# Kernel tuning notes

Measured on AMD Instinct MI355X. Metric: run time of the kernel, lower is better.

Reference implementation:

```python
import jax, jax.numpy as jnp
import numpy as np
import math

B, C, A, W, H = 8, 128, 16, 64, 64


def setup_inputs() -> dict:
    key = jax.random.key(0)
    ks = jax.random.split(key, 7)
    s_in = 1.0 / math.sqrt(C)
    return {
        "x": jax.random.normal(ks[0], (B, C, W, H), dtype=jnp.float32),
        "Wq": jax.random.normal(ks[1], (A, C), dtype=jnp.float32) * s_in,
        "bq": jnp.zeros((A,), dtype=jnp.float32),
        "Wk": jax.random.normal(ks[2], (A, C), dtype=jnp.float32) * s_in,
        "bk": jnp.zeros((A,), dtype=jnp.float32),
        "Wv": jax.random.normal(ks[3], (C, C), dtype=jnp.float32) * s_in,
        "bv": jnp.zeros((C,), dtype=jnp.float32),
    }


def reference(x, Wq, bq, Wk, bk, Wv, bv):
    # 1x1 convs == per-pixel linear projections
    q = jnp.einsum('ac,bcwh->bawh', Wq, x) + bq[None, :, None, None]  # [B,A,W,H]
    k = jnp.einsum('ac,bcwh->bawh', Wk, x) + bk[None, :, None, None]  # [B,A,W,H]
    v = jnp.einsum('vc,bcwh->bvwh', Wv, x) + bv[None, :, None, None]  # [B,C,W,H]

    scale = 1.0 / math.sqrt(q.shape[1])
    # full spatial attention: [B, W, H, W, H]
    attn = jnp.einsum('bawh,baWH->bwhWH', q, k)
    b, w, h, _, _ = attn.shape
    attn = jax.nn.softmax(attn.reshape(b, w, h, -1) * scale, axis=-1)
    attn = attn.reshape(b, w, h, w, h)
    out = jnp.einsum('bwhWH,bvWH->bvwh', attn, v)  # [B,C,W,H]
    return out
```

## Files before the change

### kernel.cpp

```cpp
#include <hip/hip_runtime.h>
#include <math.h>

#define BB 8
#define CC 128
#define NN 4096

typedef _Float16 f16;
typedef _Float16 f16x4v __attribute__((ext_vector_type(4)));
typedef _Float16 f16x8 __attribute__((ext_vector_type(8)));
typedef float f32x4v __attribute__((ext_vector_type(4)));
typedef float f32x16 __attribute__((ext_vector_type(16)));

#if __has_builtin(__builtin_amdgcn_exp2f)
#define EXP2(x) __builtin_amdgcn_exp2f(x)
#else
#define EXP2(x) __expf((x)*0.69314718056f)
#endif

#define QSCALE 0.360673760222f
#define SHIFT  5.770780163555f

#define WF_BYTES 65536

__global__ __launch_bounds__(256)
void prep_kernel(const float* __restrict__ Wq, const float* __restrict__ bq,
                 const float* __restrict__ Wk, const float* __restrict__ bk,
                 const float* __restrict__ Wv, const float* __restrict__ bv,
                 f16* __restrict__ Wf, float* __restrict__ biasS)
{
    const int tg = blockIdx.x*256 + threadIdx.x;
    if (tg < 2560) {
        const int mt = tg >> 9, ks = (tg >> 6) & 7, l = tg & 63;
        const int n32 = l & 31, h = l >> 5;
        const int r = mt*32 + n32;
        f16x8 v8;
        #pragma unroll
        for (int i = 0; i < 8; i++) {
            int c = ks*16 + 8*h + i;
            float wv_;
            if (r < 16)      wv_ = QSCALE * Wq[r*CC + c];
            else if (r < 32) wv_ = Wk[(r-16)*CC + c];
            else             wv_ = Wv[(r-32)*CC + c];
            v8[i] = (f16)wv_;
        }
        *(f16x8*)&Wf[(size_t)tg*8] = v8;
    }
    if (blockIdx.x == 0 && threadIdx.x < 160) {
        int r = threadIdx.x;
        biasS[r] = r < 16 ? QSCALE*bq[r] : (r < 32 ? bk[r-16] : bv[r-32]);
    }
}

__global__ __launch_bounds__(256)
void proj_kernel(const float* __restrict__ x, const f16* __restrict__ Wf,
                 const float* __restrict__ biasS,
                 f16* __restrict__ Qt, f16* __restrict__ Kt, f16* __restrict__ Vf)
{
    __shared__ __align__(16) f16 Vl[CC*140];

    const int tid  = threadIdx.x;
    const int lane = tid & 63;
    const int wv   = tid >> 6;
    const int b    = blockIdx.x & 7;
    const int pt   = blockIdx.x >> 3;
    const int n32  = lane & 31;
    const int half = lane >> 5;
    const int p    = pt*128 + wv*32 + n32;

    const float* xp = x + (size_t)b*CC*NN + p;
    f16x8 xf[8];
    #pragma unroll
    for (int ks = 0; ks < 8; ks++) {
        float xv[8];
        #pragma unroll
        for (int i = 0; i < 8; i++)
            xv[i] = __builtin_nontemporal_load(&xp[(size_t)(ks*16 + 8*half + i)*NN]);
        #pragma unroll
        for (int i = 0; i < 8; i++) xf[ks][i] = (f16)xv[i];
    }

    f32x16 acc[5];
    #pragma unroll
    for (int mt = 0; mt < 5; mt++) acc[mt] = (f32x16)0.0f;
    #pragma unroll
    for (int ks = 0; ks < 8; ks++) {
        #pragma unroll
        for (int mt = 0; mt < 5; mt++) {
            f16x8 wfr = *(const f16x8*)&Wf[((size_t)(mt*8 + ks)*64 + lane)*8];
            acc[mt] = __builtin_amdgcn_mfma_f32_32x32x16_f16(wfr, xf[ks], acc[mt], 0, 0, 0);
        }
    }

    #pragma unroll
    for (int mt = 0; mt < 5; mt++) {
        #pragma unroll
        for (int q = 0; q < 4; q++) {
            float4 b4 = *(const float4*)&biasS[mt*32 + q*8 + 4*half];
            acc[mt][q*4+0] += b4.x; acc[mt][q*4+1] += b4.y;
            acc[mt][q*4+2] += b4.z; acc[mt][q*4+3] += b4.w;
        }
    }

    {
        size_t qkoff = ((size_t)b*NN + p)*16;
        f16x4v s0, s1, s2, s3;
        #pragma unroll
        for (int i = 0; i < 4; i++) {
            s0[i] = (f16)acc[0][i];    s1[i] = (f16)acc[0][4+i];
            s2[i] = (f16)acc[0][8+i];  s3[i] = (f16)acc[0][12+i];
        }
        *(f16x4v*)&Qt[qkoff + 4*half]     = s0;
        *(f16x4v*)&Qt[qkoff + 8 + 4*half] = s1;
        *(f16x4v*)&Kt[qkoff + 4*half]     = s2;
        *(f16x4v*)&Kt[qkoff + 8 + 4*half] = s3;
    }

    #pragma unroll
    for (int mt = 1; mt < 5; mt++) {
        #pragma unroll
        for (int g = 0; g < 16; g++) {
            int c = (mt-1)*32 + (g & 3) + 8*(g >> 2) + 4*half;
            Vl[c*140 + wv*32 + n32] = (f16)acc[mt][g];
        }
    }
    __syncthreads();

    #pragma unroll
    for (int pass = 0; pass < 8; pass++) {
        int item = pass*256 + tid;
        int l    = item & 63;
        int f    = (item >> 6) & 15;
        int ktl  = item >> 10;
        int c16  = f >> 2, ct = f & 3;
        int li   = l & 31, h2 = l >> 5;
        const f16* src = &Vl[(ct*32 + li)*140 + ktl*64 + c16*16 + 4*h2];
        f16x4v lo = *(const f16x4v*)&src[0];
        f16x4v hi = *(const f16x4v*)&src[8];
        f16x8 v8;
        #pragma unroll
        for (int i = 0; i < 4; i++) { v8[i] = lo[i]; v8[4+i] = hi[i]; }
        int ktg = pt*2 + ktl;
        *(f16x8*)&Vf[((((size_t)b*64 + ktg)*16 + c16*4 + ct)*64 + l)*8] = v8;
    }
}

__global__ __launch_bounds__(256, 2)
void attn_kernel(const f16* __restrict__ Qt, const f16* __restrict__ Kt,
                 const f16* __restrict__ Vf, float* __restrict__ out)
{
    __shared__ __align__(16) unsigned char lds_raw[27776];

    const int tid  = threadIdx.x;
    const int lane = tid & 63;
    const int wv   = tid >> 6;
    const int b    = blockIdx.x & 7;
    const int qt   = blockIdx.x >> 3;
    const int q0   = qt*32;
    const int n32  = lane & 31;
    const int half = lane >> 5;

    const f16* vb = Vf + (size_t)b*64*16*512;
    const f16* kb = Kt + (size_t)b*NN*16;
    const f16x8 qf = *(const f16x8*)&Qt[((size_t)b*NN + q0 + n32)*16 + half*8];

    f32x16 of[4];
    #pragma unroll
    for (int ct = 0; ct < 4; ct++) of[ct] = (f32x16)0.0f;
    float ps[4] = {0.f, 0.f, 0.f, 0.f};

    f16x8 kf0 = *(const f16x8*)&kb[((size_t)wv*64 + n32)*16 + half*8];
    f16x8 kf1 = *(const f16x8*)&kb[((size_t)wv*64 + 32 + n32)*16 + half*8];
    f16x8 vpf[16];
    {
        const f16* vt = vb + (size_t)wv*8192;
        #pragma unroll
        for (int i = 0; i < 16; i++)
            vpf[i] = *(const f16x8*)&vt[((size_t)i*64 + lane)*8];
    }

    for (int kt = wv; kt < NN/64; kt += 4) {
        const int ktn = (kt + 4 < NN/64) ? kt + 4 : kt;
        f16x8 kf0n = *(const f16x8*)&kb[((size_t)ktn*64 + n32)*16 + half*8];
        f16x8 kf1n = *(const f16x8*)&kb[((size_t)ktn*64 + 32 + n32)*16 + half*8];

        f32x16 St0 = __builtin_amdgcn_mfma_f32_32x32x16_f16(kf0, qf, (f32x16)(-SHIFT), 0, 0, 0);
        f32x16 St1 = __builtin_amdgcn_mfma_f32_32x32x16_f16(kf1, qf, (f32x16)(-SHIFT), 0, 0, 0);

        f16x8 pf[4];
        #pragma unroll
        for (int g = 0; g < 16; g++) {
            float e0 = EXP2(St0[g]); ps[g & 3] += e0; pf[(g >> 3)][g & 7]     = (f16)e0;
            float e1 = EXP2(St1[g]); ps[g & 3] += e1; pf[2 + (g >> 3)][g & 7] = (f16)e1;
        }

        const f16* vtn = vb + (size_t)ktn*8192;
        #pragma unroll
        for (int kc = 0; kc < 4; kc++) {
            #pragma unroll
            for (int ct = 0; ct < 4; ct++) {
                const int i = kc*4 + ct;
                f16x8 vc = vpf[i];
                vpf[i] = *(const f16x8*)&vtn[((size_t)i*64 + lane)*8];
                of[ct] = __builtin_amdgcn_mfma_f32_32x32x16_f16(pf[kc], vc, of[ct], 0, 0, 0);
            }
        }
        kf0 = kf0n; kf1 = kf1n;
    }

    float ls = (ps[0] + ps[1]) + (ps[2] + ps[3]);
    ls += __shfl_xor(ls, 32);

    __syncthreads();
    if (wv != 0) {
        unsigned char* base = lds_raw + (size_t)(wv-1)*9216 + (size_t)lane*144;
        #pragma unroll
        for (int ct = 0; ct < 4; ct++) {
            #pragma unroll
            for (int h = 0; h < 2; h++) {
                f16x8 t;
                #pragma unroll
                for (int jj = 0; jj < 8; jj++) t[jj] = (f16)of[ct][h*8+jj];
                *(f16x8*)(base + ct*32 + h*16) = t;
            }
        }
        *(float*)(base + 128) = ls;
    }
    __syncthreads();
    if (wv == 0) {
        #pragma unroll
        for (int s2 = 0; s2 < 3; s2++) {
            unsigned char* base = lds_raw + (size_t)s2*9216 + (size_t)lane*144;
            #pragma unroll
            for (int ct = 0; ct < 4; ct++) {
                #pragma unroll
                for (int h = 0; h < 2; h++) {
                    f16x8 t = *(const f16x8*)(base + ct*32 + h*16);
                    #pragma unroll
                    for (int jj = 0; jj < 8; jj++) of[ct][h*8+jj] += (float)t[jj];
                }
            }
            ls += *(const float*)(base + 128);
        }
        float* ls_inv = (float*)(lds_raw + 27648);
        if (lane < 32) ls_inv[lane] = 1.f / ls;
        float invq[16];
        #pragma unroll
        for (int g = 0; g < 16; g++)
            invq[g] = ls_inv[(g & 3) + 8*(g >> 2) + 4*half];
        float* Tb = (float*)lds_raw;
        #pragma unroll
        for (int ct = 0; ct < 4; ct++) {
            #pragma unroll
            for (int g = 0; g < 16; g++) {
                int row = (g & 3) + 8*(g >> 2) + 4*half;
                Tb[(ct*32 + n32)*36 + row] = of[ct][g] * invq[g];
            }
        }
    }
    __syncthreads();
    {
        const float* Tb = (const float*)lds_raw;
        #pragma unroll
        for (int it = 0; it < 4; it++) {
            int idx = it*256 + tid;
            int c = idx >> 3, qq = idx & 7;
            f32x4v v = *(const f32x4v*)&Tb[c*36 + qq*4];
            __builtin_nontemporal_store(v,
                (f32x4v*)&out[((size_t)b*CC + c)*NN + q0 + qq*4]);
        }
    }
}

extern "C" void kernel_launch(void* const* d_in, const int* in_sizes, int n_in,
                              void* d_out, int out_size, void* d_ws, size_t ws_size,
                              hipStream_t stream) {
    const float* x  = (const float*)d_in[0];
    const float* Wq = (const float*)d_in[1];
    const float* bq = (const float*)d_in[2];
    const float* Wk = (const float*)d_in[3];
    const float* bk = (const float*)d_in[4];
    const float* Wv = (const float*)d_in[5];
    const float* bv = (const float*)d_in[6];
    float* out = (float*)d_out;

    f16* Qw = (f16*)d_ws;
    f16* Kw = Qw + (size_t)BB*NN*16;
    f16* Vw = Kw + (size_t)BB*NN*16;
    unsigned char* tail = (unsigned char*)d_out + (size_t)out_size*4 - WF_BYTES;
    f16*   Wf    = (f16*)tail;
    float* biasS = (float*)(tail + 49152);

    hipLaunchKernelGGL(prep_kernel, dim3(10), dim3(256), 0, stream,
                       Wq, bq, Wk, bk, Wv, bv, Wf, biasS);
    hipLaunchKernelGGL(proj_kernel, dim3(256), dim3(256), 0, stream,
                       x, Wf, biasS, Qw, Kw, Vw);
    hipLaunchKernelGGL(attn_kernel, dim3(1024), dim3(256), 0, stream,
                       Qw, Kw, Vw, out);
}
```

Measured before the change: 137.2 us.

## Software-pipeline softmax exp with PV MFMAs across key tiles

```diff
diff --git a/kernel.cpp b/kernel.cpp
--- a/kernel.cpp
+++ b/kernel.cpp
@@ -6,6 +6,7 @@
 #define NN 4096
 
 typedef _Float16 f16;
+typedef __fp16 h16x2 __attribute__((ext_vector_type(2)));
 typedef _Float16 f16x4v __attribute__((ext_vector_type(4)));
 typedef _Float16 f16x8 __attribute__((ext_vector_type(8)));
 typedef float f32x4v __attribute__((ext_vector_type(4)));
@@ -162,6 +163,7 @@
     const f16* vb = Vf + (size_t)b*64*16*512;
     const f16* kb = Kt + (size_t)b*NN*16;
     const f16x8 qf = *(const f16x8*)&Qt[((size_t)b*NN + q0 + n32)*16 + half*8];
+    const f32x16 negS = (f32x16)(-SHIFT);
 
     f32x16 of[4];
     #pragma unroll
@@ -177,23 +179,38 @@
         for (int i = 0; i < 16; i++)
             vpf[i] = *(const f16x8*)&vt[((size_t)i*64 + lane)*8];
     }
-
-    for (int kt = wv; kt < NN/64; kt += 4) {
-        const int ktn = (kt + 4 < NN/64) ? kt + 4 : kt;
-        f16x8 kf0n = *(const f16x8*)&kb[((size_t)ktn*64 + n32)*16 + half*8];
-        f16x8 kf1n = *(const f16x8*)&kb[((size_t)ktn*64 + 32 + n32)*16 + half*8];
-
-        f32x16 St0 = __builtin_amdgcn_mfma_f32_32x32x16_f16(kf0, qf, (f32x16)(-SHIFT), 0, 0, 0);
-        f32x16 St1 = __builtin_amdgcn_mfma_f32_32x32x16_f16(kf1, qf, (f32x16)(-SHIFT), 0, 0, 0);
-
-        f16x8 pf[4];
-        #pragma unroll
-        for (int g = 0; g < 16; g++) {
-            float e0 = EXP2(St0[g]); ps[g & 3] += e0; pf[(g >> 3)][g & 7]     = (f16)e0;
-            float e1 = EXP2(St1[g]); ps[g & 3] += e1; pf[2 + (g >> 3)][g & 7] = (f16)e1;
-        }
+    f16x8 pf[4];
+    {
+        f32x16 St0 = __builtin_amdgcn_mfma_f32_32x32x16_f16(kf0, qf, negS, 0, 0, 0);
+        f32x16 St1 = __builtin_amdgcn_mfma_f32_32x32x16_f16(kf1, qf, negS, 0, 0, 0);
+        kf0 = *(const f16x8*)&kb[((size_t)(wv+4)*64 + n32)*16 + half*8];
+        kf1 = *(const f16x8*)&kb[((size_t)(wv+4)*64 + 32 + n32)*16 + half*8];
+        #pragma unroll
+        for (int j = 0; j < 4; j++) {
+            float a0 = EXP2(St0[2*j]),   a1 = EXP2(St0[2*j+1]);
+            float b0 = EXP2(St0[8+2*j]), b1 = EXP2(St0[8+2*j+1]);
+            float c0 = EXP2(St1[2*j]),   c1 = EXP2(St1[2*j+1]);
+            float d0 = EXP2(St1[8+2*j]), d1 = EXP2(St1[8+2*j+1]);
+            ps[(2*j) & 3] += a0 + b0 + c0 + d0;
+            ps[(2*j+1) & 3] += a1 + b1 + c1 + d1;
+            ((h16x2*)&pf[0])[j] = __builtin_amdgcn_cvt_pkrtz(a0, a1);
+            ((h16x2*)&pf[1])[j] = __builtin_amdgcn_cvt_pkrtz(b0, b1);
+            ((h16x2*)&pf[2])[j] = __builtin_amdgcn_cvt_pkrtz(c0, c1);
+            ((h16x2*)&pf[3])[j] = __builtin_amdgcn_cvt_pkrtz(d0, d1);
+        }
+    }
+
+    for (int kt = wv; kt + 4 < NN/64; kt += 4) {
+        const int ktn  = kt + 4;
+        const int ktnn = (ktn + 4 < NN/64) ? ktn + 4 : ktn;
+
+        f32x16 St0 = __builtin_amdgcn_mfma_f32_32x32x16_f16(kf0, qf, negS, 0, 0, 0);
+        f32x16 St1 = __builtin_amdgcn_mfma_f32_32x32x16_f16(kf1, qf, negS, 0, 0, 0);
+        kf0 = *(const f16x8*)&kb[((size_t)ktnn*64 + n32)*16 + half*8];
+        kf1 = *(const f16x8*)&kb[((size_t)ktnn*64 + 32 + n32)*16 + half*8];
 
         const f16* vtn = vb + (size_t)ktn*8192;
+        f16x8 pfn[4];
         #pragma unroll
         for (int kc = 0; kc < 4; kc++) {
             #pragma unroll
@@ -203,8 +220,25 @@
                 vpf[i] = *(const f16x8*)&vtn[((size_t)i*64 + lane)*8];
                 of[ct] = __builtin_amdgcn_mfma_f32_32x32x16_f16(pf[kc], vc, of[ct], 0, 0, 0);
             }
-        }
-        kf0 = kf0n; kf1 = kf1n;
+            const int base = (kc & 1)*8;
+            #pragma unroll
+            for (int j = 0; j < 4; j++) {
+                float e0 = (kc < 2) ? EXP2(St0[base + 2*j])   : EXP2(St1[base + 2*j]);
+                float e1 = (kc < 2) ? EXP2(St0[base + 2*j+1]) : EXP2(St1[base + 2*j+1]);
+                ps[(2*j) & 3]   += e0;
+                ps[(2*j+1) & 3] += e1;
+                ((h16x2*)&pfn[kc])[j] = __builtin_amdgcn_cvt_pkrtz(e0, e1);
+            }
+        }
+        #pragma unroll
+        for (int kc = 0; kc < 4; kc++) pf[kc] = pfn[kc];
+    }
+
+    #pragma unroll
+    for (int kc = 0; kc < 4; kc++) {
+        #pragma unroll
+        for (int ct = 0; ct < 4; ct++)
+            of[ct] = __builtin_amdgcn_mfma_f32_32x32x16_f16(pf[kc], vpf[kc*4 + ct], of[ct], 0, 0, 0);
     }
 
     float ls = (ps[0] + ps[1]) + (ps[2] + ps[3]);
```

Result: no change. 138.5 us (+0.9%).
